# Performance work log

Hardware: AMD Instinct MI355X
Metric: run time of the kernel (lower is better)

The kernel has to match this reference:

```python
import jax, jax.numpy as jnp
import numpy as np

K = 20          # neighbors
EPS = 1e-5      # BatchNorm eps
SLOPE = 0.2     # LeakyReLU negative slope


def setup_inputs() -> dict:
    key = jax.random.key(0)
    ks = jax.random.split(key, 6)
    B, C, N, O = 8, 3, 4096, 64
    x = jax.random.normal(ks[0], (B, C, N), dtype=jnp.float32)
    W = jax.random.normal(ks[1], (O, 2 * C), dtype=jnp.float32) * 0.1  # conv1x1 weight, bias=False
    gamma = 1.0 + 0.1 * jax.random.normal(ks[2], (O,), dtype=jnp.float32)
    beta = 0.1 * jax.random.normal(ks[3], (O,), dtype=jnp.float32)
    mean = 0.1 * jax.random.normal(ks[4], (O,), dtype=jnp.float32)
    var = jax.random.uniform(ks[5], (O,), dtype=jnp.float32, minval=0.5, maxval=1.5)
    return {"x": x, "W": W, "gamma": gamma, "beta": beta, "mean": mean, "var": var}


def reference(x, W, gamma, beta, mean, var):
    # x: [B, C, N]
    B, C, N = x.shape
    xt = jnp.swapaxes(x, 1, 2)                                   # [B, N, C]
    xx = jnp.sum(x * x, axis=1)                                  # [B, N]
    pd = 2.0 * jnp.einsum('bnc,bmc->bnm', xt, xt) - xx[:, :, None] - xx[:, None, :]
    _, idx = jax.lax.top_k(pd, K)                                # [B, N, K] nearest neighbors
    # gather neighbor features per batch
    feat = jax.vmap(lambda f, i: f[i])(xt, idx)                  # [B, N, K, C]
    center = xt[:, :, None, :]                                   # [B, N, 1, C]
    edge = jnp.concatenate(
        [feat - center, jnp.broadcast_to(center, feat.shape)], axis=-1)  # [B, N, K, 2C]
    # 1x1 conv == channel matmul
    y = jnp.einsum('bnkc,oc->bnko', edge, W)                     # [B, N, K, O]
    inv = gamma / jnp.sqrt(var + EPS)                            # fused inference BatchNorm
    y = y * inv + (beta - mean * inv)
    y = jnp.where(y >= 0, y, SLOPE * y)                          # LeakyReLU(0.2)
    y = jnp.max(y, axis=2)                                       # max over k -> [B, N, O]
    return jnp.swapaxes(y, 1, 2)                                 # [B, O, N]
```

## Files before the change

### kernel.cpp

```cpp
#include <hip/hip_runtime.h>
#include <math.h>

#define NPTS 4096
#define KNN  20
#define NOUT 64
#define QPB  16
#define BLKT (QPB * 64)
#define POOLCAP 256

__device__ __forceinline__ unsigned ord32(float f) {
    unsigned u = __float_as_uint(f);
    int m = ((int)u) >> 31;
    return u ^ ((unsigned)m | 0x80000000u);
}

__global__ __launch_bounds__(BLKT, 4) void edgeconv_kernel(
    const float* __restrict__ x,
    const float* __restrict__ Wm,
    const float* __restrict__ gamma,
    const float* __restrict__ beta,
    const float* __restrict__ mean,
    const float* __restrict__ var,
    float* __restrict__ out)
{
    const int bid = blockIdx.x;
    const int b   = bid >> 8;
    const int n0  = (bid & 255) * QPB;
    const int t    = threadIdx.x;
    const int lane = t & 63;
    const int w    = t >> 6;

    __shared__ float4 tile[NPTS];
    __shared__ unsigned long long pool[QPB * POOLCAP];
    __shared__ int cnt[QPB];
    __shared__ float outT[NOUT * 17];

    const float* xb = x + (size_t)b * 3 * NPTS;

    if (lane == 0) cnt[w] = 0;

    #pragma unroll
    for (int k2 = 0; k2 < NPTS / BLKT; ++k2) {
        const int c = t + k2 * BLKT;
        const float a0 = xb[c];
        const float a1 = xb[NPTS + c];
        const float a2 = xb[2 * NPTS + c];
        const float sq = fmaf(a0, a0, fmaf(a1, a1, a2 * a2));
        tile[c] = make_float4(a0, a1, a2, sq);
    }
    __syncthreads();

    const int n = n0 + w;
    const float4 pv = tile[n];
    const float p0 = pv.x, p1 = pv.y, p2 = pv.z, xxp = pv.w;
    const float q0 = 2.f * p0, q1 = 2.f * p1, q2 = 2.f * p2;

    float d[64];
    float vmax = -INFINITY;
    const float4* tl = tile + lane;
    #pragma unroll
    for (int g = 0; g < 8; ++g) {
        float4 cc[8];
        #pragma unroll
        for (int u = 0; u < 8; ++u) cc[u] = tl[(g * 8 + u) * 64];
        #pragma unroll
        for (int u = 0; u < 8; ++u) {
            const float dd =
                (fmaf(q0, cc[u].x, fmaf(q1, cc[u].y, q2 * cc[u].z)) - xxp) - cc[u].w;
            d[g * 8 + u] = dd;
            vmax = fmaxf(vmax, dd);
        }
    }

    float T;
    {
        float v = vmax;
        #pragma unroll
        for (int k = 2; k <= 64; k <<= 1) {
            #pragma unroll
            for (int j = k >> 1; j > 0; j >>= 1) {
                const float o = __shfl_xor(v, j, 64);
                const bool keep_min = ((lane & j) == 0) == ((lane & k) != 0);
                v = keep_min ? fminf(v, o) : fmaxf(v, o);
            }
        }
        T = __shfl(v, 19, 64);
    }

    const int invl = (NPTS - 1) - lane;
    #pragma unroll
    for (int j = 0; j < 64; ++j) {
        if (d[j] >= T) {
            const int pos = atomicAdd(&cnt[w], 1);
            if (pos < POOLCAP)
                pool[w * POOLCAP + pos] =
                    ((unsigned long long)ord32(d[j]) << 32) |
                    (unsigned)(invl - j * 64);
        }
    }
    const int c_ = cnt[w];

    unsigned long long key = 0ull;
    if (c_ <= 64) {
        if (lane < c_) key = pool[w * POOLCAP + lane];
        #pragma unroll
        for (int k = 2; k <= 64; k <<= 1) {
            #pragma unroll
            for (int j = k >> 1; j > 0; j >>= 1) {
                const unsigned long long o = __shfl_xor(key, j, 64);
                const bool keep_min = ((lane & j) == 0) == ((lane & k) != 0);
                const unsigned long long mn = (key < o) ? key : o;
                const unsigned long long mx = (key < o) ? o : key;
                key = keep_min ? mn : mx;
            }
        }
    } else {
        const int cc2 = (c_ < POOLCAP) ? c_ : POOLCAP;
        for (int r = 0; r < KNN; ++r) {
            unsigned long long bk = 0ull; int bp = -1;
            for (int i = lane; i < cc2; i += 64) {
                const unsigned long long kk = pool[w * POOLCAP + i];
                if (kk > bk) { bk = kk; bp = i; }
            }
            unsigned long long rb = bk;
            #pragma unroll
            for (int s = 32; s > 0; s >>= 1) {
                const unsigned long long o = __shfl_xor(rb, s, 64);
                if (o > rb) rb = o;
            }
            if (bk == rb && bp >= 0) pool[w * POOLCAP + bp] = 0ull;
            if (lane == r) key = rb;
        }
    }

    const int o = lane;
    const float iv   = gamma[o] / sqrtf(var[o] + 1e-5f);
    const float bias = beta[o] - mean[o] * iv;
    const float* Wr = Wm + o * 6;
    const float w0p = Wr[0] * iv, w1p = Wr[1] * iv, w2p = Wr[2] * iv;
    const float w3p = Wr[3] * iv, w4p = Wr[4] * iv, w5p = Wr[5] * iv;
    const float basep = fmaf(w3p, p0, fmaf(w4p, p1, fmaf(w5p, p2, bias)));

    const unsigned lowb = (unsigned)(key & 0xFFFFFFFFull);
    float best = -INFINITY;
    #pragma unroll
    for (int k = 0; k < KNN; ++k) {
        const unsigned lk = (unsigned)__builtin_amdgcn_readlane((int)lowb, k);
        const int gi = (NPTS - 1) - (int)lk;
        const float4 f = tile[gi];
        float y = fmaf(w0p, f.x - p0,
                   fmaf(w1p, f.y - p1,
                    fmaf(w2p, f.z - p2, basep)));
        y = fmaxf(y, 0.2f * y);
        best = fmaxf(best, y);
    }
    outT[o * 17 + w] = best;
    __syncthreads();

    if (t < NOUT * 4) {
        const int oo = t >> 2, seg = t & 3;
        const int s4 = seg * 4;
        float4 vv;
        vv.x = outT[oo * 17 + s4 + 0];
        vv.y = outT[oo * 17 + s4 + 1];
        vv.z = outT[oo * 17 + s4 + 2];
        vv.w = outT[oo * 17 + s4 + 3];
        *(float4*)(out + ((size_t)b * NOUT + oo) * NPTS + n0 + s4) = vv;
    }
}

extern "C" void kernel_launch(void* const* d_in, const int* in_sizes, int n_in,
                              void* d_out, int out_size, void* d_ws, size_t ws_size,
                              hipStream_t stream) {
    const float* x     = (const float*)d_in[0];
    const float* Wm    = (const float*)d_in[1];
    const float* gamma = (const float*)d_in[2];
    const float* beta  = (const float*)d_in[3];
    const float* mean  = (const float*)d_in[4];
    const float* var   = (const float*)d_in[5];
    float* out = (float*)d_out;

    const int B = in_sizes[0] / (3 * NPTS);
    const int nblocks = B * (NPTS / QPB);
    edgeconv_kernel<<<nblocks, BLKT, 0, stream>>>(x, Wm, gamma, beta, mean, var, out);
}
```

Baseline: 147.9 us.

## Prepack points, halve LDS tile, ballot-based compaction and 32-bit key sort

Adds a pack kernel that writes each point as float4 with its negated squared norm into the workspace. The main kernel stages only half the points in LDS and reads the other half straight from global/L2, while block size is halved to 8 queries. Per-wave LDS atomics are replaced by ballot/mbcnt compaction, the pool capacity shrinks, and the top-k sort uses 32-bit keys with a 64-bit fallback. Neighbor features are then gathered from global memory. Together these reduce LDS footprint and staging cost to raise occupancy, at the price of more global loads and an extra launch.

```diff
diff --git a/kernel.cpp b/kernel.cpp
--- a/kernel.cpp
+++ b/kernel.cpp
@@ -4,9 +4,10 @@
 #define NPTS 4096
 #define KNN  20
 #define NOUT 64
-#define QPB  16
+#define QPB  8
 #define BLKT (QPB * 64)
-#define POOLCAP 256
+#define PCAP 96
+#define HALF 2048
 
 __device__ __forceinline__ unsigned ord32(float f) {
     unsigned u = __float_as_uint(f);
@@ -14,8 +15,22 @@
     return u ^ ((unsigned)m | 0x80000000u);
 }
 
+__device__ __forceinline__ int mbcnt64(unsigned long long m) {
+    return __builtin_amdgcn_mbcnt_hi((unsigned)(m >> 32),
+           __builtin_amdgcn_mbcnt_lo((unsigned)m, 0));
+}
+
+__global__ __launch_bounds__(256) void pack_kernel(const float* __restrict__ x,
+                                                   float4* __restrict__ xq) {
+    const int i = blockIdx.x * 256 + threadIdx.x;
+    const int b = i >> 12, j = i & (NPTS - 1);
+    const float* xb = x + (size_t)b * 3 * NPTS;
+    const float a0 = xb[j], a1 = xb[NPTS + j], a2 = xb[2 * NPTS + j];
+    xq[i] = make_float4(a0, a1, a2, -fmaf(a0, a0, fmaf(a1, a1, a2 * a2)));
+}
+
 __global__ __launch_bounds__(BLKT, 4) void edgeconv_kernel(
-    const float* __restrict__ x,
+    const float4* __restrict__ xq,
     const float* __restrict__ Wm,
     const float* __restrict__ gamma,
     const float* __restrict__ beta,
@@ -24,51 +39,52 @@
     float* __restrict__ out)
 {
     const int bid = blockIdx.x;
-    const int b   = bid >> 8;
-    const int n0  = (bid & 255) * QPB;
+    const int b   = bid >> 9;
+    const int n0  = (bid & 511) * QPB;
     const int t    = threadIdx.x;
     const int lane = t & 63;
     const int w    = t >> 6;
 
-    __shared__ float4 tile[NPTS];
-    __shared__ unsigned long long pool[QPB * POOLCAP];
-    __shared__ int cnt[QPB];
-    __shared__ float outT[NOUT * 17];
-
-    const float* xb = x + (size_t)b * 3 * NPTS;
-
-    if (lane == 0) cnt[w] = 0;
-
-    #pragma unroll
-    for (int k2 = 0; k2 < NPTS / BLKT; ++k2) {
+    __shared__ float4 tile[HALF];
+    __shared__ unsigned long long pool[QPB * PCAP];
+
+    const float4* xqb = xq + (size_t)b * NPTS;
+
+    #pragma unroll
+    for (int k2 = 0; k2 < HALF / BLKT; ++k2) {
         const int c = t + k2 * BLKT;
-        const float a0 = xb[c];
-        const float a1 = xb[NPTS + c];
-        const float a2 = xb[2 * NPTS + c];
-        const float sq = fmaf(a0, a0, fmaf(a1, a1, a2 * a2));
-        tile[c] = make_float4(a0, a1, a2, sq);
+        tile[c] = xqb[c];
     }
     __syncthreads();
 
-    const int n = n0 + w;
-    const float4 pv = tile[n];
-    const float p0 = pv.x, p1 = pv.y, p2 = pv.z, xxp = pv.w;
-    const float q0 = 2.f * p0, q1 = 2.f * p1, q2 = 2.f * p2;
+    const int nu = __builtin_amdgcn_readfirstlane(n0 + w);
+    const float4 pv = xqb[nu];
+    const float q0 = 2.f * pv.x, q1 = 2.f * pv.y, q2 = 2.f * pv.z;
 
     float d[64];
     float vmax = -INFINITY;
-    const float4* tl = tile + lane;
-    #pragma unroll
-    for (int g = 0; g < 8; ++g) {
+    #pragma unroll
+    for (int g = 0; g < 4; ++g) {
         float4 cc[8];
         #pragma unroll
-        for (int u = 0; u < 8; ++u) cc[u] = tl[(g * 8 + u) * 64];
+        for (int u = 0; u < 8; ++u) cc[u] = tile[(g * 8 + u) * 64 + lane];
         #pragma unroll
         for (int u = 0; u < 8; ++u) {
-            const float dd =
-                (fmaf(q0, cc[u].x, fmaf(q1, cc[u].y, q2 * cc[u].z)) - xxp) - cc[u].w;
-            d[g * 8 + u] = dd;
-            vmax = fmaxf(vmax, dd);
+            const float e = fmaf(q0, cc[u].x, fmaf(q1, cc[u].y, fmaf(q2, cc[u].z, cc[u].w)));
+            d[g * 8 + u] = e;
+            vmax = fmaxf(vmax, e);
+        }
+    }
+    #pragma unroll
+    for (int g = 4; g < 8; ++g) {
+        float4 cc[8];
+        #pragma unroll
+        for (int u = 0; u < 8; ++u) cc[u] = xqb[(g * 8 + u) * 64 + lane];
+        #pragma unroll
+        for (int u = 0; u < 8; ++u) {
+            const float e = fmaf(q0, cc[u].x, fmaf(q1, cc[u].y, fmaf(q2, cc[u].z, cc[u].w)));
+            d[g * 8 + u] = e;
+            vmax = fmaxf(vmax, e);
         }
     }
 
@@ -88,39 +104,65 @@
     }
 
     const int invl = (NPTS - 1) - lane;
+    int base = 0;
     #pragma unroll
     for (int j = 0; j < 64; ++j) {
-        if (d[j] >= T) {
-            const int pos = atomicAdd(&cnt[w], 1);
-            if (pos < POOLCAP)
-                pool[w * POOLCAP + pos] =
-                    ((unsigned long long)ord32(d[j]) << 32) |
-                    (unsigned)(invl - j * 64);
-        }
-    }
-    const int c_ = cnt[w];
-
-    unsigned long long key = 0ull;
-    if (c_ <= 64) {
-        if (lane < c_) key = pool[w * POOLCAP + lane];
+        const bool surv = d[j] >= T;
+        const unsigned long long mk = __ballot(surv);
+        if (mk) {
+            if (surv) {
+                const int pos = base + mbcnt64(mk);
+                if (pos < PCAP)
+                    pool[w * PCAP + pos] =
+                        ((unsigned long long)ord32(d[j]) << 32) |
+                        (unsigned)(invl - j * 64);
+            }
+            base += __popcll(mk);
+        }
+    }
+    const int cnt = (base < PCAP) ? base : PCAP;
+
+    unsigned* idxbuf = (unsigned*)(pool + (size_t)w * PCAP);
+    unsigned long long kk = 0ull;
+    if (lane < cnt) kk = pool[w * PCAP + lane];
+
+    if (cnt <= 64) {
+        const unsigned key = (unsigned)(kk >> 32);
+        unsigned v = key;
         #pragma unroll
         for (int k = 2; k <= 64; k <<= 1) {
             #pragma unroll
             for (int j = k >> 1; j > 0; j >>= 1) {
-                const unsigned long long o = __shfl_xor(key, j, 64);
+                const unsigned o = (unsigned)__shfl_xor((int)v, j, 64);
                 const bool keep_min = ((lane & j) == 0) == ((lane & k) != 0);
-                const unsigned long long mn = (key < o) ? key : o;
-                const unsigned long long mx = (key < o) ? o : key;
-                key = keep_min ? mn : mx;
-            }
+                v = keep_min ? min(v, o) : max(v, o);
+            }
+        }
+        const unsigned K20 = (unsigned)__shfl((int)v, 19, 64);
+        const unsigned long long ge = __ballot(key >= K20);
+        if (__popcll(ge) == KNN) {
+            if (key >= K20) idxbuf[mbcnt64(ge)] = (unsigned)kk;
+        } else {
+            unsigned long long key64 = kk;
+            #pragma unroll
+            for (int k = 2; k <= 64; k <<= 1) {
+                #pragma unroll
+                for (int j = k >> 1; j > 0; j >>= 1) {
+                    const unsigned long long o = __shfl_xor(key64, j, 64);
+                    const bool keep_min = ((lane & j) == 0) == ((lane & k) != 0);
+                    const unsigned long long mn = (key64 < o) ? key64 : o;
+                    const unsigned long long mx = (key64 < o) ? o : key64;
+                    key64 = keep_min ? mn : mx;
+                }
+            }
+            if (lane < KNN) idxbuf[lane] = (unsigned)key64;
         }
     } else {
-        const int cc2 = (c_ < POOLCAP) ? c_ : POOLCAP;
         for (int r = 0; r < KNN; ++r) {
             unsigned long long bk = 0ull; int bp = -1;
-            for (int i = lane; i < cc2; i += 64) {
-                const unsigned long long kk = pool[w * POOLCAP + i];
-                if (kk > bk) { bk = kk; bp = i; }
+            for (int i = lane; i < cnt; i += 64) {
+                const unsigned long long e = pool[w * PCAP + i];
+                if (e > bk) { bk = e; bp = i; }
             }
             unsigned long long rb = bk;
             #pragma unroll
@@ -128,10 +170,14 @@
                 const unsigned long long o = __shfl_xor(rb, s, 64);
                 if (o > rb) rb = o;
             }
-            if (bk == rb && bp >= 0) pool[w * POOLCAP + bp] = 0ull;
-            if (lane == r) key = rb;
-        }
-    }
+            if (bk == rb && bp >= 0) pool[w * PCAP + bp] = 0ull;
+            if (lane == 0) idxbuf[r] = (unsigned)rb;
+        }
+    }
+
+    const unsigned myidx = idxbuf[(lane < KNN) ? lane : 0];
+
+    __syncthreads();
 
     const int o = lane;
     const float iv   = gamma[o] / sqrtf(var[o] + 1e-5f);
@@ -139,33 +185,32 @@
     const float* Wr = Wm + o * 6;
     const float w0p = Wr[0] * iv, w1p = Wr[1] * iv, w2p = Wr[2] * iv;
     const float w3p = Wr[3] * iv, w4p = Wr[4] * iv, w5p = Wr[5] * iv;
-    const float basep = fmaf(w3p, p0, fmaf(w4p, p1, fmaf(w5p, p2, bias)));
-
-    const unsigned lowb = (unsigned)(key & 0xFFFFFFFFull);
+    const float basep = fmaf(w3p, pv.x, fmaf(w4p, pv.y, fmaf(w5p, pv.z, bias)));
+
     float best = -INFINITY;
     #pragma unroll
     for (int k = 0; k < KNN; ++k) {
-        const unsigned lk = (unsigned)__builtin_amdgcn_readlane((int)lowb, k);
-        const int gi = (NPTS - 1) - (int)lk;
-        const float4 f = tile[gi];
-        float y = fmaf(w0p, f.x - p0,
-                   fmaf(w1p, f.y - p1,
-                    fmaf(w2p, f.z - p2, basep)));
+        const int lk = __builtin_amdgcn_readlane((int)myidx, k);
+        const int gi = __builtin_amdgcn_readfirstlane((NPTS - 1) - lk);
+        const float4 f = xqb[gi];
+        float y = fmaf(w0p, f.x - pv.x,
+                   fmaf(w1p, f.y - pv.y,
+                    fmaf(w2p, f.z - pv.z, basep)));
         y = fmaxf(y, 0.2f * y);
         best = fmaxf(best, y);
     }
-    outT[o * 17 + w] = best;
+
+    float* outT = (float*)pool;
+    outT[o * 9 + w] = best;
     __syncthreads();
 
-    if (t < NOUT * 4) {
-        const int oo = t >> 2, seg = t & 3;
-        const int s4 = seg * 4;
+    if (t < NOUT * 2) {
+        const int oo = t >> 1, seg = t & 1;
+        const int sb = oo * 9 + seg * 4;
         float4 vv;
-        vv.x = outT[oo * 17 + s4 + 0];
-        vv.y = outT[oo * 17 + s4 + 1];
-        vv.z = outT[oo * 17 + s4 + 2];
-        vv.w = outT[oo * 17 + s4 + 3];
-        *(float4*)(out + ((size_t)b * NOUT + oo) * NPTS + n0 + s4) = vv;
+        vv.x = outT[sb + 0]; vv.y = outT[sb + 1];
+        vv.z = outT[sb + 2]; vv.w = outT[sb + 3];
+        *(float4*)(out + ((size_t)b * NOUT + oo) * NPTS + n0 + seg * 4) = vv;
     }
 }
 
@@ -179,8 +224,10 @@
     const float* mean  = (const float*)d_in[4];
     const float* var   = (const float*)d_in[5];
     float* out = (float*)d_out;
+    float4* xq = (float4*)d_ws;
 
     const int B = in_sizes[0] / (3 * NPTS);
+    pack_kernel<<<B * NPTS / 256, 256, 0, stream>>>(x, xq);
     const int nblocks = B * (NPTS / QPB);
-    edgeconv_kernel<<<nblocks, BLKT, 0, stream>>>(x, Wm, gamma, beta, mean, var, out);
-}
+    edgeconv_kernel<<<nblocks, BLKT, 0, stream>>>(xq, Wm, gamma, beta, mean, var, out);
+}
```

After: 144.8 us. -2.1%, faster.
